# Performance work log

Measured on AMD Instinct MI355X. Metric: run time of the kernel, lower is better.

Reference implementation:

```python
import jax, jax.numpy as jnp
import numpy as np
import math

B, S, D, H, DK = 2, 4096, 512, 8, 64

def setup_inputs() -> dict:
    key = jax.random.key(0)
    ks = jax.random.split(key, 11)
    scale = 1.0 / math.sqrt(D)
    inp = {
        'q': jax.random.normal(ks[0], (B, S, D), jnp.float32),
        'k': jax.random.normal(ks[1], (B, S, D), jnp.float32),
        'v': jax.random.normal(ks[2], (B, S, D), jnp.float32),
        # causal mask: True = masked (as consumed by masked_fill)
        'mask': jnp.triu(jnp.ones((S, S), jnp.bool_), k=1)[None, None, :, :],
        'wq': jax.random.normal(ks[3], (D, D), jnp.float32) * scale,
        'bq': jnp.zeros((D,), jnp.float32),
        'wk': jax.random.normal(ks[4], (D, D), jnp.float32) * scale,
        'bk': jnp.zeros((D,), jnp.float32),
        'wv': jax.random.normal(ks[5], (D, D), jnp.float32) * scale,
        'bv': jnp.zeros((D,), jnp.float32),
        'wo': jax.random.normal(ks[6], (D, D), jnp.float32) * scale,
        'bo': jnp.zeros((D,), jnp.float32),
    }
    return inp

def reference(q, k, v, mask, wq, bq, wk, bk, wv, bv, wo, bo):
    # torch nn.Linear: y = x @ W^T + b
    def proj(x, w, b):
        return x @ w.T + b
    def heads(x):  # [B,S,D] -> [B,H,S,DK]
        return x.reshape(B, S, H, DK).transpose(0, 2, 1, 3)
    qh = heads(proj(q, wq, bq))
    kh = heads(proj(k, wk, bk))
    vh = heads(proj(v, wv, bv))
    scores = jnp.einsum('bhqd,bhkd->bhqk', qh, kh) / math.sqrt(DK)
    # NOTE: faithful to source, masked positions are filled with -1e-09 (not -inf)
    scores = jnp.where(mask, jnp.float32(-1e-09), scores)
    attn = jax.nn.softmax(scores, axis=-1)
    x = jnp.einsum('bhqk,bhkd->bhqd', attn, vh)
    x = x.transpose(0, 2, 1, 3).reshape(B, S, D)
    return proj(x, wo, bo)
```

## Files before the change

### kernel.cpp

```cpp
#include <hip/hip_runtime.h>
#include <math.h>

#define SS 4096
#define DD 512
#define HH 8
#define DKK 64

#define MSUB 4.0f
#define W_MASK 0.0183156393f
#define CST 136

typedef _Float16 half8_t __attribute__((ext_vector_type(8)));
typedef _Float16 half4_t __attribute__((ext_vector_type(4)));
typedef float f32x4 __attribute__((ext_vector_type(4)));
typedef float f32x16 __attribute__((ext_vector_type(16)));

__device__ __forceinline__ f32x4 mfma16(half8_t a, half8_t b, f32x4 c) {
    return __builtin_amdgcn_mfma_f32_16x16x32_f16(a, b, c, 0, 0, 0);
}
__device__ __forceinline__ f32x16 mfma32(half8_t a, half8_t b, f32x16 c) {
    return __builtin_amdgcn_mfma_f32_32x32x16_f16(a, b, c, 0, 0, 0);
}
__device__ __forceinline__ f32x16 zero16() {
    f32x16 z;
#pragma unroll
    for (int i = 0; i < 16; i++) z[i] = 0.f;
    return z;
}
__device__ __forceinline__ void gld_lds16(const _Float16* g, _Float16* l) {
    __builtin_amdgcn_global_load_lds((const __attribute__((address_space(1))) void*)g,
                                     (__attribute__((address_space(3))) void*)l, 16, 0, 0);
}

__global__ __launch_bounds__(256) void cvt_prep(
    const float* __restrict__ q, const float* __restrict__ k, const float* __restrict__ v,
    const float* __restrict__ wq, const float* __restrict__ wk,
    const float* __restrict__ wv, const float* __restrict__ wo,
    _Float16* qf, _Float16* kf, _Float16* vf,
    _Float16* wqf, _Float16* wkf, _Float16* wvf, _Float16* wof)
{
    const float* srcs[7] = {q, k, v, wq, wk, wv, wo};
    _Float16* dsts[7] = {qf, kf, vf, wqf, wkf, wvf, wof};
    const int ns[7] = {4194304, 4194304, 4194304, 262144, 262144, 262144, 262144};
    int t = blockIdx.y;
    size_t i0 = ((size_t)blockIdx.x * 256 + threadIdx.x) * 8;
    if (i0 >= (size_t)ns[t]) return;
    const float* s = srcs[t];
    _Float16* d = dsts[t];
    float4 a = *(const float4*)(s + i0);
    float4 b = *(const float4*)(s + i0 + 4);
    half8_t h = {(_Float16)a.x, (_Float16)a.y, (_Float16)a.z, (_Float16)a.w,
                 (_Float16)b.x, (_Float16)b.y, (_Float16)b.z, (_Float16)b.w};
    *(half8_t*)(d + i0) = h;
}

__global__ __launch_bounds__(256, 3) void gemm_qkv(
    const _Float16* __restrict__ qf, const _Float16* __restrict__ kf,
    const _Float16* __restrict__ vf,
    const _Float16* __restrict__ wqf, const _Float16* __restrict__ wkf,
    const _Float16* __restrict__ wvf,
    const float* __restrict__ bq, const float* __restrict__ bk,
    const float* __restrict__ bv,
    _Float16* __restrict__ Qf, _Float16* __restrict__ Kf,
    _Float16* __restrict__ Vf, _Float16* __restrict__ Vt)
{
    __shared__ __align__(16) _Float16 smem[17408];
    const int z = blockIdx.z;
    const _Float16* A = z == 0 ? qf : (z == 1 ? kf : vf);
    const _Float16* W = z == 0 ? wqf : (z == 1 ? wkf : wvf);
    const float* bias = z == 0 ? bq : (z == 1 ? bk : bv);

    const int tid = threadIdx.x;
    const int w = tid >> 6, lane = tid & 63, q = lane >> 4, cc = lane & 15;
    const int h5 = lane >> 5, l31 = lane & 31;
    const int mtile = blockIdx.x * 128, ntile = blockIdx.y * 128;
    const int mw = (w & 1) * 64, nw = (w >> 1) * 64;
    const int srow = lane >> 3, scol = (lane & 7) * 8;

    f32x4 acc[4][4];
#pragma unroll
    for (int i = 0; i < 4; i++)
#pragma unroll
        for (int j = 0; j < 4; j++) {
            f32x4 zf = {0.f, 0.f, 0.f, 0.f};
            acc[i][j] = zf;
        }

    for (int kt = 0; kt < 512; kt += 64) {
        __syncthreads();
#pragma unroll
        for (int i = 0; i < 4; i++) {
            int r0 = w * 32 + i * 8;
            gld_lds16(A + (size_t)(mtile + r0 + srow) * 512 + kt + scol, &smem[r0 * 64]);
            gld_lds16(W + (size_t)(ntile + r0 + srow) * 512 + kt + scol, &smem[8192 + r0 * 64]);
        }
        __syncthreads();
#pragma unroll
        for (int kh = 0; kh < 2; kh++) {
            half8_t ar[4], br[4];
#pragma unroll
            for (int i = 0; i < 4; i++)
                ar[i] = *(const half8_t*)(&smem[(mw + i * 16 + cc) * 64 + kh * 32 + q * 8]);
#pragma unroll
            for (int j = 0; j < 4; j++)
                br[j] = *(const half8_t*)(&smem[8192 + (nw + j * 16 + cc) * 64 + kh * 32 + q * 8]);
#pragma unroll
            for (int i = 0; i < 4; i++)
#pragma unroll
                for (int j = 0; j < 4; j++)
                    acc[i][j] = mfma16(ar[i], br[j], acc[i][j]);
        }
    }

    const int b = mtile >> 12;
    const int ms = mtile & 4095;

    __syncthreads();
#pragma unroll
    for (int jb = 0; jb < 4; jb++) {
        int nloc = nw + jb * 16 + cc;
        int n = ntile + nloc;
        float bvv = bias[n];
#pragma unroll
        for (int it = 0; it < 4; it++) {
            int mloc = mw + it * 16 + q * 4;
            half4_t pk;
#pragma unroll
            for (int r = 0; r < 4; r++) {
                _Float16 hv = (_Float16)(acc[it][jb][r] + bvv);
                pk[r] = hv;
                smem[(mloc + r) * CST + nloc] = hv;
            }
            if (z == 2) {
                int bh = b * 8 + (n >> 6);
                int dkl = n & 63;
                *(half4_t*)(Vt + ((size_t)bh * 64 + dkl) * SS + ms + mloc) = pk;
            }
        }
    }
    __syncthreads();

    if (z == 0) {
#pragma unroll
        for (int i = 0; i < 8; i++) {
            int e = w * 8 + i;
            int s5 = e >> 3, hh = (e >> 2) & 1, d4 = e & 3;
            int row = s5 * 32 + l31;
            int col = hh * 64 + d4 * 16 + h5 * 8;
            half8_t vv = *(const half8_t*)(&smem[row * CST + col]);
            int bh = b * 8 + (ntile >> 6) + hh;
            size_t base = ((size_t)(bh * 128 + (ms >> 5) + s5) * 4 + d4) * 512;
            *(half8_t*)(Qf + base + lane * 8) = vv;
        }
    } else if (z == 1) {
#pragma unroll
        for (int i = 0; i < 8; i++) {
            int e = w * 8 + i;
            int s6 = e >> 4, s5b = (e >> 3) & 1, hh = (e >> 2) & 1, d4 = e & 3;
            int row = s6 * 64 + s5b * 32 + l31;
            int col = hh * 64 + d4 * 16 + h5 * 8;
            half8_t vv = *(const half8_t*)(&smem[row * CST + col]);
            int bh = b * 8 + (ntile >> 6) + hh;
            size_t base = ((size_t)(bh * 64 + (ms >> 6) + s6) * 8 + s5b * 4 + d4) * 512;
            *(half8_t*)(Kf + base + lane * 8) = vv;
        }
    } else {
#pragma unroll
        for (int i = 0; i < 8; i++) {
            int e = w * 8 + i;
            int s6 = e >> 4, c = (e >> 2) & 3, hh = (e >> 1) & 1, d5 = e & 1;
            int col = hh * 64 + d5 * 32 + l31;
            half8_t vv;
#pragma unroll
            for (int k0 = 0; k0 < 8; k0++) {
                int mrow = s6 * 64 + c * 16 + (k0 & 3) + 4 * h5 + 8 * (k0 >> 2);
                vv[k0] = smem[mrow * CST + col];
            }
            int bh = b * 8 + (ntile >> 6) + hh;
            size_t base = ((size_t)(bh * 64 + (ms >> 6) + s6) * 8 + c * 2 + d5) * 512;
            *(half8_t*)(Vf + base + lane * 8) = vv;
        }
    }
}

__global__ __launch_bounds__(256) void suffix_v(const _Float16* __restrict__ Vt,
                                                _Float16* __restrict__ SufVt)
{
    __shared__ float csum[4][65];
    const int bh = blockIdx.x >> 4;
    const int dk = (blockIdx.x & 15) * 4 + (threadIdx.x >> 6);
    const int dki = threadIdx.x >> 6;
    const int c = threadIdx.x & 63;
    const _Float16* vp = Vt + ((size_t)bh * 64 + dk) * SS + c * 64;

    half8_t v8[8];
    float acc = 0.f;
#pragma unroll
    for (int j = 0; j < 8; j++) {
        v8[j] = *(const half8_t*)(vp + j * 8);
#pragma unroll
        for (int t = 0; t < 8; t++) acc += (float)v8[j][t];
    }
    csum[dki][c] = acc;
    __syncthreads();
    if (threadIdx.x < 4) {
        float a = 0.f;
        for (int c2 = 63; c2 >= 0; c2--) {
            float t2 = csum[threadIdx.x][c2];
            csum[threadIdx.x][c2] = a;
            a += t2;
        }
    }
    __syncthreads();
    float a = csum[dki][c];
    _Float16* op = SufVt + ((size_t)bh * 64 + dk) * SS + c * 64;
#pragma unroll
    for (int j = 7; j >= 0; j--) {
        half8_t o8;
#pragma unroll
        for (int t = 7; t >= 0; t--) {
            o8[t] = (_Float16)a;
            a += (float)v8[j][t];
        }
        *(half8_t*)(op + j * 8) = o8;
    }
}

__device__ __forceinline__ void exp_pack(const f32x16& s, half8_t& pa, half8_t& pb,
                                         float& lsum) {
#pragma unroll
    for (int i = 0; i < 16; i++) {
        float p = __expf(fmaf(s[i], 0.125f, -MSUB));
        lsum += p;
        if (i < 8) pa[i] = (_Float16)p; else pb[i - 8] = (_Float16)p;
    }
}
__device__ __forceinline__ void exp_pack_mask(const f32x16& s, int j0, int mg, int h5,
                                              half8_t& pa, half8_t& pb, float& lsum) {
#pragma unroll
    for (int i = 0; i < 16; i++) {
        int jg = j0 + (i & 3) + 8 * (i >> 2) + 4 * h5;
        float p = __expf(fmaf(s[i], 0.125f, -MSUB));
        if (jg > mg) p = 0.f;
        lsum += p;
        if (i < 8) pa[i] = (_Float16)p; else pb[i - 8] = (_Float16)p;
    }
}

__global__ __launch_bounds__(256, 2) void attn_part(
    const _Float16* __restrict__ Qf, const _Float16* __restrict__ Kf,
    const _Float16* __restrict__ Vf,
    _Float16* __restrict__ Opart, float* __restrict__ Lp)
{
    static const int t_qb[30] = {15,15,15,14,14,14,13,13,13,12,12,12,11,11,
                                 10,10,9,9,8,8,7,7,6,6,5,4,3,2,1,0};
    static const int t_c0[30] = {0,22,43, 0,20,40, 0,19,38, 0,18,35, 0,24,
                                 0,22, 0,20, 0,18, 0,16, 0,14, 0, 0, 0, 0, 0, 0};
    static const int t_nt[30] = {22,21,21,20,20,20,19,19,18,18,17,17,24,24,
                                 22,22,20,20,18,18,16,16,14,14,24,20,16,12,8,4};

    __shared__ __align__(16) _Float16 lds[16384];
    const int tid = threadIdx.x;
    const int w = tid >> 6, lane = tid & 63;
    const int h5 = lane >> 5, l31 = lane & 31;
    const int bh = blockIdx.x & 15;
    const int tix = blockIdx.x >> 4;
    const int qb = t_qb[tix], c0 = t_c0[tix], NT = t_nt[tix];
    const int qbaseA = qb * 256 + w * 64;
    const int tdw = qb * 4 + w;
    const int mgA = qbaseA + l31, mgB = qbaseA + 32 + l31;
    const int qgA = qb * 8 + w * 2;

    const _Float16* qpA = Qf + ((size_t)(bh * 128 + qgA)) * 2048 + lane * 8;
    half8_t qA[4], qB[4];
#pragma unroll
    for (int s = 0; s < 4; s++) {
        qA[s] = *(const half8_t*)(qpA + s * 512);
        qB[s] = *(const half8_t*)(qpA + 2048 + s * 512);
    }

    const _Float16* Kb = Kf + (size_t)bh * 262144 + lane * 8;
    const _Float16* Vb = Vf + (size_t)bh * 262144 + lane * 8;

    f32x16 oA0 = zero16(), oA1 = zero16(), oB0 = zero16(), oB1 = zero16();
    float lsA = 0.f, lsB = 0.f;

    {
        const _Float16* kg = Kb + (size_t)c0 * 4096;
        const _Float16* vg = Vb + (size_t)c0 * 4096;
        gld_lds16(kg + (2 * w) * 512,     &lds[(2 * w) * 512]);
        gld_lds16(kg + (2 * w + 1) * 512, &lds[(2 * w + 1) * 512]);
        gld_lds16(vg + (2 * w) * 512,     &lds[4096 + (2 * w) * 512]);
        gld_lds16(vg + (2 * w + 1) * 512, &lds[4096 + (2 * w + 1) * 512]);
    }

    for (int t = 0; t < NT; t++) {
        const int p = (t & 1) * 8192;
        __syncthreads();
        if (t + 1 < NT) {
            const int p2 = 8192 - p;
            const _Float16* kg = Kb + (size_t)(c0 + t + 1) * 4096;
            const _Float16* vg = Vb + (size_t)(c0 + t + 1) * 4096;
            gld_lds16(kg + (2 * w) * 512,     &lds[p2 + (2 * w) * 512]);
            gld_lds16(kg + (2 * w + 1) * 512, &lds[p2 + (2 * w + 1) * 512]);
            gld_lds16(vg + (2 * w) * 512,     &lds[p2 + 4096 + (2 * w) * 512]);
            gld_lds16(vg + (2 * w + 1) * 512, &lds[p2 + 4096 + (2 * w + 1) * 512]);
        }
        const int jblk = c0 + t;
        if (jblk <= tdw) {
            const bool dg = (jblk == tdw);
            const _Float16* Lk = &lds[p];
            const _Float16* Lv = &lds[p + 4096];
            half8_t pa, pb;
            {
                f32x16 s0 = zero16();
#pragma unroll
                for (int s = 0; s < 4; s++)
                    s0 = mfma32(*(const half8_t*)(Lk + s * 512 + lane * 8), qA[s], s0);
                if (dg) exp_pack_mask(s0, jblk * 64, mgA, h5, pa, pb, lsA);
                else    exp_pack(s0, pa, pb, lsA);
                oA0 = mfma32(pa, *(const half8_t*)(Lv + 0 * 512 + lane * 8), oA0);
                oA1 = mfma32(pa, *(const half8_t*)(Lv + 1 * 512 + lane * 8), oA1);
                oA0 = mfma32(pb, *(const half8_t*)(Lv + 2 * 512 + lane * 8), oA0);
                oA1 = mfma32(pb, *(const half8_t*)(Lv + 3 * 512 + lane * 8), oA1);
                if (!dg) {
                    f32x16 s1 = zero16();
#pragma unroll
                    for (int s = 0; s < 4; s++)
                        s1 = mfma32(*(const half8_t*)(Lk + (4 + s) * 512 + lane * 8), qA[s], s1);
                    exp_pack(s1, pa, pb, lsA);
                    oA0 = mfma32(pa, *(const half8_t*)(Lv + 4 * 512 + lane * 8), oA0);
                    oA1 = mfma32(pa, *(const half8_t*)(Lv + 5 * 512 + lane * 8), oA1);
                    oA0 = mfma32(pb, *(const half8_t*)(Lv + 6 * 512 + lane * 8), oA0);
                    oA1 = mfma32(pb, *(const half8_t*)(Lv + 7 * 512 + lane * 8), oA1);
                }
            }
            {
                f32x16 s2 = zero16();
#pragma unroll
                for (int s = 0; s < 4; s++)
                    s2 = mfma32(*(const half8_t*)(Lk + s * 512 + lane * 8), qB[s], s2);
                exp_pack(s2, pa, pb, lsB);
                oB0 = mfma32(pa, *(const half8_t*)(Lv + 0 * 512 + lane * 8), oB0);
                oB1 = mfma32(pa, *(const half8_t*)(Lv + 1 * 512 + lane * 8), oB1);
                oB0 = mfma32(pb, *(const half8_t*)(Lv + 2 * 512 + lane * 8), oB0);
                oB1 = mfma32(pb, *(const half8_t*)(Lv + 3 * 512 + lane * 8), oB1);
                f32x16 s3 = zero16();
#pragma unroll
                for (int s = 0; s < 4; s++)
                    s3 = mfma32(*(const half8_t*)(Lk + (4 + s) * 512 + lane * 8), qB[s], s3);
                if (dg) exp_pack_mask(s3, jblk * 64 + 32, mgB, h5, pa, pb, lsB);
                else    exp_pack(s3, pa, pb, lsB);
                oB0 = mfma32(pa, *(const half8_t*)(Lv + 4 * 512 + lane * 8), oB0);
                oB1 = mfma32(pa, *(const half8_t*)(Lv + 5 * 512 + lane * 8), oB1);
                oB0 = mfma32(pb, *(const half8_t*)(Lv + 6 * 512 + lane * 8), oB0);
                oB1 = mfma32(pb, *(const half8_t*)(Lv + 7 * 512 + lane * 8), oB1);
            }
        }
    }
    __syncthreads();

    lsA += __shfl_xor(lsA, 32);
    lsB += __shfl_xor(lsB, 32);
    const size_t task = (size_t)bh * 30 + tix;
    if (h5 == 0) {
        Lp[task * 256 + w * 64 + l31] = lsA;
        Lp[task * 256 + w * 64 + 32 + l31] = lsB;
    }

#pragma unroll
    for (int r = 0; r < 16; r++) {
        int row = (r & 3) + 8 * (r >> 2) + 4 * h5;
        lds[(w * 64 + row) * 64 + l31]            = (_Float16)oA0[r];
        lds[(w * 64 + row) * 64 + 32 + l31]       = (_Float16)oA1[r];
        lds[(w * 64 + 32 + row) * 64 + l31]       = (_Float16)oB0[r];
        lds[(w * 64 + 32 + row) * 64 + 32 + l31]  = (_Float16)oB1[r];
    }
    __syncthreads();
    _Float16* Op = Opart + task * 16384;
#pragma unroll
    for (int i = 0; i < 8; i++)
        *(half8_t*)(Op + i * 2048 + tid * 8) = *(const half8_t*)(&lds[i * 2048 + tid * 8]);
}

__global__ __launch_bounds__(256) void attn_reduce(
    const _Float16* __restrict__ Opart, const float* __restrict__ Lp,
    const _Float16* __restrict__ SufVt, _Float16* __restrict__ X)
{
    static const int r_n[16]  = {1,1,1,1,1,1,2,2,2,2,2,2,3,3,3,3};
    static const int r_f0[16] = {29,28,27,26,25,24,22,20,18,16,14,12,9,6,3,0};
    __shared__ __align__(16) _Float16 sfv[16384];
    __shared__ float linv[256];
    const int t = threadIdx.x;
    const int bh = blockIdx.x & 15, qb = blockIdx.x >> 4;
    const int n = r_n[qb];
    const size_t f0 = (size_t)bh * 30 + r_f0[qb];

    const int dk = t & 63, sblk = t >> 6;
#pragma unroll
    for (int i = 0; i < 8; i++) {
        half8_t sv = *(const half8_t*)(SufVt + ((size_t)bh * 64 + dk) * SS
                                       + qb * 256 + sblk * 64 + i * 8);
#pragma unroll
        for (int j = 0; j < 8; j++)
            sfv[(sblk * 64 + i * 8 + j) * 64 + dk] = sv[j];
    }
    {
        float l = 0.f;
        for (int c = 0; c < n; c++) l += Lp[(f0 + c) * 256 + t];
        linv[t] = 1.f / (l + (float)(SS - 1 - qb * 256 - t) * W_MASK);
    }
    __syncthreads();

    const int b = bh >> 3, hh = bh & 7;
#pragma unroll
    for (int i = 0; i < 8; i++) {
        int e = i * 2048 + t * 8;
        int row = e >> 6;
        float iv = linv[row];
        float acc[8] = {0.f, 0.f, 0.f, 0.f, 0.f, 0.f, 0.f, 0.f};
        for (int c = 0; c < n; c++) {
            half8_t o8 = *(const half8_t*)(Opart + (f0 + c) * 16384 + e);
#pragma unroll
            for (int j = 0; j < 8; j++) acc[j] += (float)o8[j];
        }
        half8_t sv8 = *(const half8_t*)(&sfv[e]);
        half8_t out8;
#pragma unroll
        for (int j = 0; j < 8; j++)
            out8[j] = (_Float16)((acc[j] + W_MASK * (float)sv8[j]) * iv);
        int s = qb * 256 + row;
        *(half8_t*)(X + ((size_t)b * SS + s) * DD + hh * 64 + (e & 63)) = out8;
    }
}

__global__ __launch_bounds__(256, 4) void gemm_out(
    const _Float16* __restrict__ A, const _Float16* __restrict__ W,
    const float* __restrict__ bias, float* __restrict__ Cout)
{
    __shared__ __align__(16) _Float16 smem[12288];
    const int tid = threadIdx.x;
    const int w = tid >> 6, lane = tid & 63, q = lane >> 4, cc = lane & 15;
    const int mtile = blockIdx.x * 128, ntile = blockIdx.y * 64;
    const int mw = (w & 1) * 64, nw = (w >> 1) * 32;
    const int srow = lane >> 3, scol = (lane & 7) * 8;

    f32x4 acc[4][2];
#pragma unroll
    for (int i = 0; i < 4; i++)
#pragma unroll
        for (int j = 0; j < 2; j++) {
            f32x4 zf = {0.f, 0.f, 0.f, 0.f};
            acc[i][j] = zf;
        }

    for (int kt = 0; kt < 512; kt += 64) {
        __syncthreads();
#pragma unroll
        for (int i = 0; i < 4; i++) {
            int r0 = w * 32 + i * 8;
            gld_lds16(A + (size_t)(mtile + r0 + srow) * 512 + kt + scol, &smem[r0 * 64]);
        }
#pragma unroll
        for (int i = 0; i < 2; i++) {
            int r0 = w * 16 + i * 8;
            gld_lds16(W + (size_t)(ntile + r0 + srow) * 512 + kt + scol, &smem[8192 + r0 * 64]);
        }
        __syncthreads();
#pragma unroll
        for (int kh = 0; kh < 2; kh++) {
            half8_t ar[4], br[2];
#pragma unroll
            for (int i = 0; i < 4; i++)
                ar[i] = *(const half8_t*)(&smem[(mw + i * 16 + cc) * 64 + kh * 32 + q * 8]);
#pragma unroll
            for (int j = 0; j < 2; j++)
                br[j] = *(const half8_t*)(&smem[8192 + (nw + j * 16 + cc) * 64 + kh * 32 + q * 8]);
#pragma unroll
            for (int i = 0; i < 4; i++)
#pragma unroll
                for (int j = 0; j < 2; j++)
                    acc[i][j] = mfma16(ar[i], br[j], acc[i][j]);
        }
    }

#pragma unroll
    for (int j = 0; j < 2; j++) {
        int coln = ntile + nw + j * 16 + cc;
        float bvv = bias[coln];
#pragma unroll
        for (int i = 0; i < 4; i++) {
            int m0 = mtile + mw + i * 16 + q * 4;
#pragma unroll
            for (int r = 0; r < 4; r++)
                Cout[(size_t)(m0 + r) * 512 + coln] = acc[i][j][r] + bvv;
        }
    }
}

extern "C" void kernel_launch(void* const* d_in, const int* in_sizes, int n_in,
                              void* d_out, int out_size, void* d_ws, size_t ws_size,
                              hipStream_t stream) {
    const float* q  = (const float*)d_in[0];
    const float* k  = (const float*)d_in[1];
    const float* v  = (const float*)d_in[2];
    const float* wq = (const float*)d_in[4];
    const float* bq = (const float*)d_in[5];
    const float* wk = (const float*)d_in[6];
    const float* bk = (const float*)d_in[7];
    const float* wv = (const float*)d_in[8];
    const float* bv = (const float*)d_in[9];
    const float* wo = (const float*)d_in[10];
    const float* bo = (const float*)d_in[11];
    float* out = (float*)d_out;

    char* ws = (char*)d_ws;
    const size_t MB = (size_t)1024 * 1024;
    _Float16* qf  = (_Float16*)(ws);
    _Float16* kf  = (_Float16*)(ws + 8 * MB);
    _Float16* vf  = (_Float16*)(ws + 16 * MB);
    _Float16* wqf = (_Float16*)(ws + 24 * MB);
    _Float16* wkf = (_Float16*)(ws + 24 * MB + 512 * 1024);
    _Float16* wvf = (_Float16*)(ws + 25 * MB);
    _Float16* wof = (_Float16*)(ws + 25 * MB + 512 * 1024);
    _Float16* Qfr = (_Float16*)(ws + 26 * MB);
    _Float16* Kfr = (_Float16*)(ws + 34 * MB);
    _Float16* Vfr = (_Float16*)(ws + 42 * MB);
    _Float16* Vt  = (_Float16*)(ws + 50 * MB);
    _Float16* Opart = (_Float16*)(ws);
    float*    Lp    = (float*)(ws + 15 * MB);
    _Float16* SufVt = vf;
    _Float16* Xa    = Vt;

    hipLaunchKernelGGL(cvt_prep, dim3(2048, 7), dim3(256), 0, stream,
                       q, k, v, wq, wk, wv, wo, qf, kf, vf, wqf, wkf, wvf, wof);
    hipLaunchKernelGGL(gemm_qkv, dim3(64, 4, 3), dim3(256), 0, stream,
                       qf, kf, vf, wqf, wkf, wvf, bq, bk, bv, Qfr, Kfr, Vfr, Vt);
    hipLaunchKernelGGL(suffix_v, dim3(256), dim3(256), 0, stream, Vt, SufVt);
    hipLaunchKernelGGL(attn_part, dim3(480), dim3(256), 0, stream,
                       Qfr, Kfr, Vfr, Opart, Lp);
    hipLaunchKernelGGL(attn_reduce, dim3(256), dim3(256), 0, stream,
                       Opart, Lp, SufVt, Xa);
    hipLaunchKernelGGL(gemm_out, dim3(64, 8), dim3(256), 0, stream, Xa, wof, bo, out);
}
```

Measured before the change: 255.9 us.

## Rebalance causal attention split into 46 finer chunks at 3 blocks per CU

Splits the causal attention work into 46 chunks per batch-head instead of 30, with roughly equal tile counts of about 12 to 15 KV tiles each, and raises launch bounds occupancy from 2 to 3 blocks per CU. This launches 736 blocks so the 256 CUs are filled more evenly with less tail imbalance. Partial outputs no longer fit in the old workspace region, so they are split across two buffers and the reduce kernel reads up to 5 partials per query block. Costs include more partial writes and reads, plus register pressure from the higher occupancy target, which could cause spills.

```diff
diff --git a/kernel.cpp b/kernel.cpp
--- a/kernel.cpp
+++ b/kernel.cpp
@@ -9,6 +9,7 @@
 #define MSUB 4.0f
 #define W_MASK 0.0183156393f
 #define CST 136
+#define NCH 46
 
 typedef _Float16 half8_t __attribute__((ext_vector_type(8)));
 typedef _Float16 half4_t __attribute__((ext_vector_type(4)));
@@ -247,17 +248,24 @@
     }
 }
 
-__global__ __launch_bounds__(256, 2) void attn_part(
+__global__ __launch_bounds__(256, 3) void attn_part(
     const _Float16* __restrict__ Qf, const _Float16* __restrict__ Kf,
     const _Float16* __restrict__ Vf,
-    _Float16* __restrict__ Opart, float* __restrict__ Lp)
+    _Float16* __restrict__ OpA, _Float16* __restrict__ OpB,
+    float* __restrict__ Lp)
 {
-    static const int t_qb[30] = {15,15,15,14,14,14,13,13,13,12,12,12,11,11,
-                                 10,10,9,9,8,8,7,7,6,6,5,4,3,2,1,0};
-    static const int t_c0[30] = {0,22,43, 0,20,40, 0,19,38, 0,18,35, 0,24,
-                                 0,22, 0,20, 0,18, 0,16, 0,14, 0, 0, 0, 0, 0, 0};
-    static const int t_nt[30] = {22,21,21,20,20,20,19,19,18,18,17,17,24,24,
-                                 22,22,20,20,18,18,16,16,14,14,24,20,16,12,8,4};
+    static const int t_qb[NCH] = {10,10,10, 13,13,13,13, 12,12,12,12,
+                                  15,15,15,15,15, 9,9,9, 11,11,11,11,
+                                  14,14,14,14,14, 8,8,8, 5,5, 2,
+                                  7,7,7, 4,4, 6,6,6, 3,3, 1, 0};
+    static const int t_c0[NCH] = {0,15,30, 0,14,28,42, 0,13,26,39,
+                                  0,13,26,39,52, 0,14,27, 0,12,24,36,
+                                  0,12,24,36,48, 0,12,24, 0,12, 0,
+                                  0,11,22, 0,10, 0,10,19, 0,8, 0, 0};
+    static const int t_nt[NCH] = {15,15,14, 14,14,14,14, 13,13,13,13,
+                                  13,13,13,13,12, 14,13,13, 12,12,12,12,
+                                  12,12,12,12,12, 12,12,12, 12,12, 12,
+                                  11,11,10, 10,10, 10,9,9, 8,8, 8, 4};
 
     __shared__ __align__(16) _Float16 lds[16384];
     const int tid = threadIdx.x;
@@ -362,10 +370,10 @@
 
     lsA += __shfl_xor(lsA, 32);
     lsB += __shfl_xor(lsB, 32);
-    const size_t task = (size_t)bh * 30 + tix;
+    const int slot = bh * NCH + tix;
     if (h5 == 0) {
-        Lp[task * 256 + w * 64 + l31] = lsA;
-        Lp[task * 256 + w * 64 + 32 + l31] = lsB;
+        Lp[slot * 256 + w * 64 + l31] = lsA;
+        Lp[slot * 256 + w * 64 + 32 + l31] = lsB;
     }
 
 #pragma unroll
@@ -377,24 +385,26 @@
         lds[(w * 64 + 32 + row) * 64 + 32 + l31]  = (_Float16)oB1[r];
     }
     __syncthreads();
-    _Float16* Op = Opart + task * 16384;
+    _Float16* Op = (slot < 512) ? (OpA + (size_t)slot * 16384)
+                                : (OpB + (size_t)(slot - 512) * 16384);
 #pragma unroll
     for (int i = 0; i < 8; i++)
         *(half8_t*)(Op + i * 2048 + tid * 8) = *(const half8_t*)(&lds[i * 2048 + tid * 8]);
 }
 
 __global__ __launch_bounds__(256) void attn_reduce(
-    const _Float16* __restrict__ Opart, const float* __restrict__ Lp,
-    const _Float16* __restrict__ SufVt, _Float16* __restrict__ X)
+    const _Float16* __restrict__ OpA, const _Float16* __restrict__ OpB,
+    const float* __restrict__ Lp, const _Float16* __restrict__ SufVt,
+    _Float16* __restrict__ X)
 {
-    static const int r_n[16]  = {1,1,1,1,1,1,2,2,2,2,2,2,3,3,3,3};
-    static const int r_f0[16] = {29,28,27,26,25,24,22,20,18,16,14,12,9,6,3,0};
+    static const int r_n[16]  = {1,1,1,2,2,2,3,3,3,3,3,4,4,4,5,5};
+    static const int r_f0[16] = {45,44,33,42,37,31,39,34,28,16,0,19,7,3,23,11};
     __shared__ __align__(16) _Float16 sfv[16384];
     __shared__ float linv[256];
     const int t = threadIdx.x;
     const int bh = blockIdx.x & 15, qb = blockIdx.x >> 4;
     const int n = r_n[qb];
-    const size_t f0 = (size_t)bh * 30 + r_f0[qb];
+    const int f0 = bh * NCH + r_f0[qb];
 
     const int dk = t & 63, sblk = t >> 6;
 #pragma unroll
@@ -420,7 +430,10 @@
         float iv = linv[row];
         float acc[8] = {0.f, 0.f, 0.f, 0.f, 0.f, 0.f, 0.f, 0.f};
         for (int c = 0; c < n; c++) {
-            half8_t o8 = *(const half8_t*)(Opart + (f0 + c) * 16384 + e);
+            int slot = f0 + c;
+            const _Float16* Op = (slot < 512) ? (OpA + (size_t)slot * 16384)
+                                              : (OpB + (size_t)(slot - 512) * 16384);
+            half8_t o8 = *(const half8_t*)(Op + e);
 #pragma unroll
             for (int j = 0; j < 8; j++) acc[j] += (float)o8[j];
         }
@@ -527,19 +540,20 @@
     _Float16* Kfr = (_Float16*)(ws + 34 * MB);
     _Float16* Vfr = (_Float16*)(ws + 42 * MB);
     _Float16* Vt  = (_Float16*)(ws + 50 * MB);
-    _Float16* Opart = (_Float16*)(ws);
-    float*    Lp    = (float*)(ws + 15 * MB);
+    _Float16* OpA = (_Float16*)(ws);
+    _Float16* OpB = (_Float16*)(ws + 50 * MB);
+    float*    Lp  = (float*)(ws + 57 * MB);
     _Float16* SufVt = vf;
-    _Float16* Xa    = Vt;
+    _Float16* Xa    = Qfr;
 
     hipLaunchKernelGGL(cvt_prep, dim3(2048, 7), dim3(256), 0, stream,
                        q, k, v, wq, wk, wv, wo, qf, kf, vf, wqf, wkf, wvf, wof);
     hipLaunchKernelGGL(gemm_qkv, dim3(64, 4, 3), dim3(256), 0, stream,
                        qf, kf, vf, wqf, wkf, wvf, bq, bk, bv, Qfr, Kfr, Vfr, Vt);
     hipLaunchKernelGGL(suffix_v, dim3(256), dim3(256), 0, stream, Vt, SufVt);
-    hipLaunchKernelGGL(attn_part, dim3(480), dim3(256), 0, stream,
-                       Qfr, Kfr, Vfr, Opart, Lp);
+    hipLaunchKernelGGL(attn_part, dim3(736), dim3(256), 0, stream,
+                       Qfr, Kfr, Vfr, OpA, OpB, Lp);
     hipLaunchKernelGGL(attn_reduce, dim3(256), dim3(256), 0, stream,
-                       Opart, Lp, SufVt, Xa);
+                       OpA, OpB, Lp, SufVt, Xa);
     hipLaunchKernelGGL(gemm_out, dim3(64, 8), dim3(256), 0, stream, Xa, wof, bo, out);
 }
```

Result: slower. 263.8 us (+3.1%).
